# Optimization experiments

Hardware: AMD Instinct MI355X
Metric: run time of the kernel (lower is better)

## Reference

```python
import jax, jax.numpy as jnp
import numpy as np

L, H, D, DH, F = 2, 12, 768, 64, 3072
B, T = 2, 2048
LN_EPS = 1e-5


def setup_inputs() -> dict:
    key = jax.random.key(0)
    ks = jax.random.split(key, 16)
    s = 0.02
    inp = {
        "x": jax.random.normal(ks[0], (B, T, D), dtype=jnp.float32),
        "attn_mask": jnp.ones((1, T, T), dtype=jnp.int32),
        # per-layer, per-head QKV projections
        "Wq": jax.random.normal(ks[1], (L, H, D, DH), jnp.float32) * s,
        "bq": jnp.zeros((L, H, DH), jnp.float32),
        "Wk": jax.random.normal(ks[2], (L, H, D, DH), jnp.float32) * s,
        "bk": jnp.zeros((L, H, DH), jnp.float32),
        "Wv": jax.random.normal(ks[3], (L, H, D, DH), jnp.float32) * s,
        "bv": jnp.zeros((L, H, DH), jnp.float32),
        # output projection over concatenated heads
        "Wo": jax.random.normal(ks[4], (L, H * DH, D), jnp.float32) * s,
        "bo": jnp.zeros((L, D), jnp.float32),
        # FFN: LayerNorm -> Linear -> GELU -> Linear
        "ln_g": jnp.ones((L, D), jnp.float32),
        "ln_b": jnp.zeros((L, D), jnp.float32),
        "W1": jax.random.normal(ks[5], (L, D, F), jnp.float32) * s,
        "b1": jnp.zeros((L, F), jnp.float32),
        "W2": jax.random.normal(ks[6], (L, F, D), jnp.float32) * s,
        "b2": jnp.zeros((L, D), jnp.float32),
    }
    return inp


def _layer(x, mask, Wq, bq, Wk, bk, Wv, bv, Wo, bo, ln_g, ln_b, W1, b1, W2, b2):
    # batched multi-head attention (equivalent to per-head loop in source)
    q = jnp.einsum("btd,hde->bhte", x, Wq) + bq[None, :, None, :]
    k = jnp.einsum("btd,hde->bhte", x, Wk) + bk[None, :, None, :]
    v = jnp.einsum("btd,hde->bhte", x, Wv) + bv[None, :, None, :]
    scores = jnp.einsum("bhte,bhse->bhts", q, k) / np.sqrt(DH).astype(np.float32)
    scores = jnp.where(mask[:, None, :, :] == 0, -jnp.inf, scores)
    alpha = jax.nn.softmax(scores, axis=-1)
    attn = jnp.einsum("bhts,bhse->bhte", alpha, v)  # [B,H,T,DH]
    concat = attn.transpose(0, 2, 1, 3).reshape(x.shape[0], x.shape[1], H * DH)
    x = concat @ Wo + bo + x  # attention residual
    # FFN with pre-LayerNorm inside the block, residual around it
    mu = jnp.mean(x, axis=-1, keepdims=True)
    var = jnp.mean(jnp.square(x - mu), axis=-1, keepdims=True)
    h = (x - mu) * jax.lax.rsqrt(var + LN_EPS) * ln_g + ln_b
    h = jax.nn.gelu(h @ W1 + b1, approximate=False) @ W2 + b2
    return h + x


def reference(x, attn_mask, Wq, bq, Wk, bk, Wv, bv, Wo, bo, ln_g, ln_b, W1, b1, W2, b2):
    for l in range(L):
        x = _layer(x, attn_mask,
                   Wq[l], bq[l], Wk[l], bk[l], Wv[l], bv[l],
                   Wo[l], bo[l], ln_g[l], ln_b[l],
                   W1[l], b1[l], W2[l], b2[l])
    return x
```

## Files before the change

### kernel.cpp

```cpp
#include <hip/hip_runtime.h>
#include <math.h>

#define CL 2
#define CH 12
#define CD 768
#define CDH 64
#define CF 3072
#define CB 2
#define CT 2048
#define CBTCD ((size_t)CB * CT * CD)

typedef __bf16 bf16x8 __attribute__((ext_vector_type(8)));
typedef float f32x4 __attribute__((ext_vector_type(4)));
typedef short s16x4 __attribute__((ext_vector_type(4)));
typedef ushort u16x4 __attribute__((ext_vector_type(4)));

#define QSCALE 0.18033688011112042f

__device__ __forceinline__ ushort f2bf(float f) {
  return __builtin_bit_cast(ushort, (__bf16)f);
}

__device__ __forceinline__ float fexp2(float x) {
  float r;
  asm volatile("v_exp_f32 %0, %1" : "=v"(r) : "v"(x));
  return r;
}

__device__ __forceinline__ float wred_sum(float v) {
#pragma unroll
  for (int o = 32; o > 0; o >>= 1) v += __shfl_xor(v, o);
  return v;
}

__device__ __forceinline__ void gload16(const ushort* g, ushort* l) {
  __builtin_amdgcn_global_load_lds(
      (const __attribute__((address_space(1))) unsigned int*)g,
      (__attribute__((address_space(3))) unsigned int*)l, 16, 0, 0);
}

enum { EPI_BF16 = 1, EPI_BIAS_BF16 = 2, EPI_BIAS_GELU_BF16 = 3, EPI_BIAS_RES_F32 = 4, EPI_BIAS_RES_F32_BF16 = 5, EPI_PART_F32 = 6 };

template <int EPI>
__global__ __launch_bounds__(256) void gemm_k(
    const ushort* __restrict__ A, int lda,
    const ushort* __restrict__ B, int ldb,
    void* __restrict__ Cv, int ldc,
    int K,
    const float* __restrict__ bias,
    const float* __restrict__ res,
    ushort* __restrict__ C2) {
  __shared__ ushort As[2][128 * 32];
  __shared__ ushort Bs[2][128 * 32];
  const int tid = threadIdx.x;
  const int lane = tid & 63;
  const int wave = tid >> 6;
  const int wm = (wave >> 1) * 64;
  const int wn = (wave & 1) * 64;

  const int gx = gridDim.x;
  const int nwg = gx * gridDim.y;
  int wgid = blockIdx.y * gx + blockIdx.x;
  const int cpx = nwg >> 3;
  wgid = (wgid & 7) * cpx + (wgid >> 3);
  const int m0 = (wgid / gx) * 128;
  const int n0 = (wgid % gx) * 128;

  const int lr = lane & 15;
  const int lg = lane >> 4;
  f32x4 acc[4][4] = {};

  const int kz = blockIdx.z * K;
  const ushort* pa = A + (size_t)(m0 + (tid >> 2)) * lda + (tid & 3) * 8 + kz;
  const ushort* pb = B + (size_t)(n0 + (tid >> 2)) * ldb + (tid & 3) * 8 + kz;

  auto stage = [&](int buf, int k0) {
#pragma unroll
    for (int p = 0; p < 2; ++p) {
      gload16(pa + (size_t)p * 64 * lda + k0, &As[buf][wave * 512 + p * 2048]);
      gload16(pb + (size_t)p * 64 * ldb + k0, &Bs[buf][wave * 512 + p * 2048]);
    }
  };

  const int nt = K >> 5;
  stage(0, 0);
  for (int kt = 0; kt < nt; ++kt) {
    const int cur = kt & 1;
    if (kt + 1 < nt) {
      stage(cur ^ 1, (kt + 1) << 5);
      asm volatile("s_waitcnt vmcnt(4)" ::: "memory");
    } else {
      asm volatile("s_waitcnt vmcnt(0)" ::: "memory");
    }
    __builtin_amdgcn_s_barrier();
    __builtin_amdgcn_sched_barrier(0);

    bf16x8 af[4], bfr[4];
#pragma unroll
    for (int f = 0; f < 4; ++f) af[f] = *(const bf16x8*)(&As[cur][(wm + f * 16 + lr) * 32 + lg * 8]);
#pragma unroll
    for (int f = 0; f < 4; ++f) bfr[f] = *(const bf16x8*)(&Bs[cur][(wn + f * 16 + lr) * 32 + lg * 8]);
#pragma unroll
    for (int i = 0; i < 4; ++i)
#pragma unroll
      for (int j = 0; j < 4; ++j)
        acc[i][j] = __builtin_amdgcn_mfma_f32_16x16x32_bf16(af[i], bfr[j], acc[i][j], 0, 0, 0);

    __builtin_amdgcn_sched_barrier(0);
    __builtin_amdgcn_s_barrier();
  }

  const int cr0 = lg * 4;
#pragma unroll
  for (int i = 0; i < 4; ++i) {
#pragma unroll
    for (int j = 0; j < 4; ++j) {
      int col = n0 + wn + j * 16 + lr;
#pragma unroll
      for (int r = 0; r < 4; ++r) {
        int row = m0 + wm + i * 16 + cr0 + r;
        float val = acc[i][j][r];
        size_t offc = (size_t)row * ldc + col;
        if constexpr (EPI == EPI_BF16) {
          ((ushort*)Cv)[offc] = f2bf(val);
        } else if constexpr (EPI == EPI_BIAS_BF16) {
          ((ushort*)Cv)[offc] = f2bf(val + bias[col]);
        } else if constexpr (EPI == EPI_BIAS_GELU_BF16) {
          float x = val + bias[col];
          float gel = 0.5f * x * (1.0f + erff(x * 0.70710678118654752f));
          ((ushort*)Cv)[offc] = f2bf(gel);
        } else if constexpr (EPI == EPI_BIAS_RES_F32) {
          ((float*)Cv)[offc] = val + bias[col] + res[offc];
        } else if constexpr (EPI == EPI_PART_F32) {
          ((float*)Cv)[blockIdx.z * CBTCD + offc] = val;
        } else {
          float o = val + bias[col] + res[offc];
          ((float*)Cv)[offc] = o;
          C2[offc] = f2bf(o);
        }
      }
    }
  }
}

template <bool DUAL>
__global__ __launch_bounds__(256) void reduce2_k(const float* __restrict__ part,
                                                 const float* __restrict__ bias,
                                                 const float* __restrict__ res,
                                                 float* __restrict__ outf,
                                                 ushort* __restrict__ outb) {
  int i = blockIdx.x * 256 + threadIdx.x;
  float4 p0 = ((const float4*)part)[i];
  float4 p1 = ((const float4*)(part + CBTCD))[i];
  float4 rr = ((const float4*)res)[i];
  int col = (i * 4) % CD;
  float4 bb = *(const float4*)(bias + col);
  float4 o;
  o.x = p0.x + p1.x + rr.x + bb.x;
  o.y = p0.y + p1.y + rr.y + bb.y;
  o.z = p0.z + p1.z + rr.z + bb.z;
  o.w = p0.w + p1.w + rr.w + bb.w;
  ((float4*)outf)[i] = o;
  if constexpr (DUAL) {
    ushort4 u;
    u.x = f2bf(o.x); u.y = f2bf(o.y); u.z = f2bf(o.z); u.w = f2bf(o.w);
    ((ushort4*)outb)[i] = u;
  }
}

__global__ __launch_bounds__(256) void flash_k(const ushort* __restrict__ qkv,
                                               const ushort* __restrict__ vt,
                                               const unsigned* __restrict__ mbits,
                                               ushort* __restrict__ out) {
  const int q0 = blockIdx.x * 64;
  const int bh = blockIdx.y;
  const int b = bh / CH, h = bh % CH;
  const int tid = threadIdx.x;
  const int lane = tid & 63;
  const int wave = tid >> 6;
  const int lr = lane & 15;
  const int lg = lane >> 4;

  __shared__ ushort Ks[64][72];
  __shared__ ushort Vt[64][72];

  const int qg = q0 + wave * 16 + lr;
  const ushort* qrow = qkv + ((size_t)(b * CT) + qg) * 2304 + h * CDH;
  bf16x8 aq0 = *(const bf16x8*)(qrow + lg * 8);
  bf16x8 aq1 = *(const bf16x8*)(qrow + 32 + lg * 8);

  f32x4 acc[4] = {};
  float m_run = -1e30f, l_run = 0.f;

  const ushort* kbase = qkv + (size_t)(b * CT) * 2304 + CD + h * CDH;
  const ushort* vbase = vt + (size_t)bh * 64 * CT;

  for (int kv0 = 0; kv0 < CT; kv0 += 64) {
    __syncthreads();
#pragma unroll
    for (int p = 0; p < 2; ++p) {
      int i = p * 2048 + tid * 8;
      int r = i >> 6, c = i & 63;
      *(bf16x8*)(&Ks[r][c]) = *(const bf16x8*)(kbase + (size_t)(kv0 + r) * 2304 + c);
      *(bf16x8*)(&Vt[r][c]) = *(const bf16x8*)(vbase + (size_t)r * CT + kv0 + c);
    }
    __syncthreads();

    f32x4 st[4];
    __builtin_amdgcn_s_setprio(1);
#pragma unroll
    for (int j = 0; j < 4; ++j) {
      bf16x8 kf0 = *(const bf16x8*)(&Ks[j * 16 + lr][lg * 8]);
      bf16x8 kf1 = *(const bf16x8*)(&Ks[j * 16 + lr][32 + lg * 8]);
      f32x4 t = {};
      t = __builtin_amdgcn_mfma_f32_16x16x32_bf16(kf0, aq0, t, 0, 0, 0);
      t = __builtin_amdgcn_mfma_f32_16x16x32_bf16(kf1, aq1, t, 0, 0, 0);
      st[j] = t;
    }
    __builtin_amdgcn_s_setprio(0);

    unsigned w0 = mbits[(size_t)qg * 64 + (kv0 >> 5)];
    unsigned w1 = mbits[(size_t)qg * 64 + (kv0 >> 5) + 1];
    float tmax = -INFINITY;
    if ((w0 & w1) == 0xFFFFFFFFu) {
#pragma unroll
      for (int j = 0; j < 4; ++j)
#pragma unroll
        for (int r = 0; r < 4; ++r) tmax = fmaxf(tmax, st[j][r]);
    } else {
#pragma unroll
      for (int j = 0; j < 4; ++j) {
        unsigned w = (j < 2) ? w0 : w1;
#pragma unroll
        for (int r = 0; r < 4; ++r) {
          int bit = (j * 16 + lg * 4 + r) & 31;
          if (((w >> bit) & 1u) == 0u) st[j][r] = -INFINITY;
          tmax = fmaxf(tmax, st[j][r]);
        }
      }
    }
    tmax = fmaxf(tmax, __shfl_xor(tmax, 16));
    tmax = fmaxf(tmax, __shfl_xor(tmax, 32));

    if (__any(tmax - m_run > 8.0f)) {
      float mnew = fmaxf(m_run, tmax);
      float sc = fexp2(m_run - mnew);
      m_run = mnew;
      l_run *= sc;
#pragma unroll
      for (int jj = 0; jj < 4; ++jj) {
        acc[jj][0] *= sc; acc[jj][1] *= sc; acc[jj][2] *= sc; acc[jj][3] *= sc;
      }
    }

    float tsum = 0.f;
    s16x4 pf[4];
#pragma unroll
    for (int j = 0; j < 4; ++j) {
      s16x4 pv;
#pragma unroll
      for (int r = 0; r < 4; ++r) {
        float p = fexp2(st[j][r] - m_run);
        tsum += p;
        pv[r] = (short)f2bf(p);
      }
      pf[j] = pv;
    }
    tsum += __shfl_xor(tsum, 16);
    tsum += __shfl_xor(tsum, 32);
    l_run += tsum;

    __builtin_amdgcn_s_setprio(1);
#pragma unroll
    for (int jj = 0; jj < 4; ++jj) {
#pragma unroll
      for (int j = 0; j < 4; ++j) {
        s16x4 vf = *(const s16x4*)(&Vt[jj * 16 + lr][j * 16 + lg * 4]);
        acc[jj] = __builtin_amdgcn_mfma_f32_16x16x16bf16_1k(vf, pf[j], acc[jj], 0, 0, 0);
      }
    }
    __builtin_amdgcn_s_setprio(0);
  }

  float inv = 1.0f / l_run;
  const int orow = b * CT + qg;
#pragma unroll
  for (int jj = 0; jj < 4; ++jj) {
    u16x4 o;
#pragma unroll
    for (int r = 0; r < 4; ++r) o[r] = f2bf(acc[jj][r] * inv);
    *(u16x4*)(out + (size_t)orow * CD + h * CDH + jj * 16 + lg * 4) = o;
  }
}

__global__ __launch_bounds__(256) void vtrans_k(const ushort* __restrict__ qkv,
                                                ushort* __restrict__ vt) {
  const int t0 = blockIdx.x * 64;
  const int bh = blockIdx.y;
  const int b = bh / CH, h = bh % CH;
  const int tid = threadIdx.x;
  __shared__ ushort tile[64][72];
#pragma unroll
  for (int p = 0; p < 2; ++p) {
    int i = p * 2048 + tid * 8;
    int tr = i >> 6, c = i & 63;
    *(bf16x8*)(&tile[tr][c]) =
        *(const bf16x8*)(qkv + (size_t)(b * CT + t0 + tr) * 2304 + 2 * CD + h * CDH + c);
  }
  __syncthreads();
#pragma unroll
  for (int p = 0; p < 2; ++p) {
    int i = p * 2048 + tid * 8;
    int er = i >> 6, tc = i & 63;
    ushort tmp[8];
#pragma unroll
    for (int j = 0; j < 8; ++j) tmp[j] = tile[tc + j][er];
    *(bf16x8*)(vt + (size_t)bh * 64 * CT + (size_t)er * CT + t0 + tc) = *(bf16x8*)tmp;
  }
}

__global__ void maskbits_k(const int* __restrict__ mask, unsigned* __restrict__ mbits) {
  int idx = blockIdx.x * 256 + threadIdx.x;
  if (idx >= CT * 64) return;
  const int* mp = mask + (size_t)(idx >> 6) * CT + (idx & 63) * 32;
  unsigned bits = 0;
#pragma unroll
  for (int j = 0; j < 32; ++j) bits |= (mp[j] != 0 ? 1u : 0u) << j;
  mbits[idx] = bits;
}

__global__ __launch_bounds__(256) void ln_k(const float* __restrict__ X,
                                            ushort* __restrict__ H,
                                            const float* __restrict__ g,
                                            const float* __restrict__ b) {
  const int t = blockIdx.x;
  const int tid = threadIdx.x;
  const float* row = X + (size_t)t * CD;
  float x0 = row[tid], x1 = row[tid + 256], x2 = row[tid + 512];
  float s = wred_sum(x0 + x1 + x2);
  __shared__ float sh[4], sh2[4];
  if ((tid & 63) == 0) sh[tid >> 6] = s;
  __syncthreads();
  float mu = (sh[0] + sh[1] + sh[2] + sh[3]) * (1.0f / 768.0f);
  float d0 = x0 - mu, d1 = x1 - mu, d2 = x2 - mu;
  float vs = wred_sum(d0 * d0 + d1 * d1 + d2 * d2);
  if ((tid & 63) == 0) sh2[tid >> 6] = vs;
  __syncthreads();
  float var = (sh2[0] + sh2[1] + sh2[2] + sh2[3]) * (1.0f / 768.0f);
  float r = 1.0f / sqrtf(var + 1e-5f);
  H[(size_t)t * CD + tid] = f2bf(d0 * r * g[tid] + b[tid]);
  H[(size_t)t * CD + tid + 256] = f2bf(d1 * r * g[tid + 256] + b[tid + 256]);
  H[(size_t)t * CD + tid + 512] = f2bf(d2 * r * g[tid + 512] + b[tid + 512]);
}

__global__ void f32_to_bf16_k(const float* __restrict__ in, ushort* __restrict__ out, int n4) {
  int i = blockIdx.x * 256 + threadIdx.x;
  if (i >= n4) return;
  float4 f = *(const float4*)(in + (size_t)i * 4);
  ushort4 u;
  u.x = f2bf(f.x); u.y = f2bf(f.y); u.z = f2bf(f.z); u.w = f2bf(f.w);
  *(ushort4*)(out + (size_t)i * 4) = u;
}

__global__ __launch_bounds__(256) void tcvt_k(const float* __restrict__ src, size_t sbs,
                                              ushort* __restrict__ dst, size_t dbs,
                                              int R, int C, float scale) {
  __shared__ float t[32][33];
  const float* s = src + blockIdx.z * sbs;
  ushort* d = dst + blockIdx.z * dbs;
  const int tx = threadIdx.x & 31;
  const int ty4 = (threadIdx.x >> 5) * 4;
  const int r0 = blockIdx.y * 32, c0 = blockIdx.x * 32;
#pragma unroll
  for (int i = 0; i < 4; ++i) t[ty4 + i][tx] = s[(size_t)(r0 + ty4 + i) * C + c0 + tx];
  __syncthreads();
#pragma unroll
  for (int i = 0; i < 4; ++i)
    d[(size_t)(c0 + ty4 + i) * R + r0 + tx] = f2bf(t[tx][ty4 + i] * scale);
}

__global__ void repack_bqkv_k(const float* __restrict__ bq, const float* __restrict__ bk,
                              const float* __restrict__ bv, float* __restrict__ dst) {
  int idx = blockIdx.x * 256 + threadIdx.x;
  if (idx >= CL * 2304) return;
  int l = idx / 2304;
  int c = idx % 2304;
  int sec = c / CD;
  int within = c % CD;
  int h = within / CDH;
  int e = within % CDH;
  const float* B = (sec == 0) ? bq : ((sec == 1) ? bk : bv);
  float v = B[((size_t)l * CH + h) * CDH + e];
  if (sec == 0) v *= QSCALE;
  dst[idx] = v;
}

extern "C" void kernel_launch(void* const* d_in, const int* in_sizes, int n_in,
                              void* d_out, int out_size, void* d_ws, size_t ws_size,
                              hipStream_t stream) {
  (void)in_sizes; (void)n_in; (void)out_size; (void)ws_size;
  const float* X = (const float*)d_in[0];
  const int* MSK = (const int*)d_in[1];
  const float* Wq = (const float*)d_in[2];
  const float* bq = (const float*)d_in[3];
  const float* Wk = (const float*)d_in[4];
  const float* bk = (const float*)d_in[5];
  const float* Wv = (const float*)d_in[6];
  const float* bv = (const float*)d_in[7];
  const float* Wo = (const float*)d_in[8];
  const float* bo = (const float*)d_in[9];
  const float* lng = (const float*)d_in[10];
  const float* lnb = (const float*)d_in[11];
  const float* W1 = (const float*)d_in[12];
  const float* b1 = (const float*)d_in[13];
  const float* W2 = (const float*)d_in[14];
  const float* b2 = (const float*)d_in[15];

  char* base = (char*)d_ws;
  size_t off = 0;
  auto alloc = [&](size_t bytes) {
    char* p = base + off;
    off = (off + bytes + 255) & ~(size_t)255;
    return p;
  };
  ushort* wqkv_t = (ushort*)alloc((size_t)CL * 2304 * CD * 2);
  ushort* wo_t = (ushort*)alloc((size_t)CL * CD * CD * 2);
  ushort* w1_t = (ushort*)alloc((size_t)CL * CF * CD * 2);
  ushort* w2_t = (ushort*)alloc((size_t)CL * CD * CF * 2);
  float* bqkv = (float*)alloc((size_t)CL * 2304 * 4);
  ushort* xb = (ushort*)alloc((size_t)CB * CT * CD * 2);
  ushort* qkv = (ushort*)alloc((size_t)CB * CT * 2304 * 2);
  ushort* vt = (ushort*)alloc((size_t)CB * CH * CDH * CT * 2);
  unsigned* mbits = (unsigned*)alloc((size_t)CT * 64 * 4);
  ushort* attno = (ushort*)alloc((size_t)CB * CT * CD * 2);
  float* xattn = (float*)alloc((size_t)CB * CT * CD * 4);
  float* xf = (float*)alloc((size_t)CB * CT * CD * 4);
  ushort* hln = (ushort*)alloc((size_t)CB * CT * CD * 2);
  ushort* gbuf = (ushort*)alloc((size_t)CB * CT * CF * 2);
  float* part = (float*)qkv;

  const int BT_ = CB * CT;

  for (int l = 0; l < CL; ++l) {
    tcvt_k<<<dim3(CDH / 32, CD / 32, CH), 256, 0, stream>>>(
        Wq + (size_t)l * CH * CD * CDH, (size_t)CD * CDH,
        wqkv_t + (size_t)l * 2304 * CD + 0 * CD * CD, (size_t)CDH * CD,
        CD, CDH, QSCALE);
    tcvt_k<<<dim3(CDH / 32, CD / 32, CH), 256, 0, stream>>>(
        Wk + (size_t)l * CH * CD * CDH, (size_t)CD * CDH,
        wqkv_t + (size_t)l * 2304 * CD + 1 * CD * CD, (size_t)CDH * CD,
        CD, CDH, 1.0f);
    tcvt_k<<<dim3(CDH / 32, CD / 32, CH), 256, 0, stream>>>(
        Wv + (size_t)l * CH * CD * CDH, (size_t)CD * CDH,
        wqkv_t + (size_t)l * 2304 * CD + 2 * CD * CD, (size_t)CDH * CD,
        CD, CDH, 1.0f);
  }
  tcvt_k<<<dim3(CD / 32, CD / 32, CL), 256, 0, stream>>>(
      Wo, (size_t)CD * CD, wo_t, (size_t)CD * CD, CD, CD, 1.0f);
  tcvt_k<<<dim3(CF / 32, CD / 32, CL), 256, 0, stream>>>(
      W1, (size_t)CD * CF, w1_t, (size_t)CF * CD, CD, CF, 1.0f);
  tcvt_k<<<dim3(CD / 32, CF / 32, CL), 256, 0, stream>>>(
      W2, (size_t)CF * CD, w2_t, (size_t)CD * CF, CF, CD, 1.0f);
  {
    int n = CL * 2304;
    repack_bqkv_k<<<(n + 255) / 256, 256, 0, stream>>>(bq, bk, bv, bqkv);
  }
  maskbits_k<<<(CT * 64 + 255) / 256, 256, 0, stream>>>(MSK, mbits);

  {
    int n4 = BT_ * CD / 4;
    f32_to_bf16_k<<<(n4 + 255) / 256, 256, 0, stream>>>(X, xb, n4);
  }

  for (int l = 0; l < CL; ++l) {
    const float* xcur = (l == 0) ? X : xf;
    gemm_k<EPI_BIAS_BF16><<<dim3(2304 / 128, BT_ / 128), 256, 0, stream>>>(
        xb, CD, wqkv_t + (size_t)l * 2304 * CD, CD, qkv, 2304, CD,
        bqkv + (size_t)l * 2304, nullptr, nullptr);
    vtrans_k<<<dim3(CT / 64, CB * CH), 256, 0, stream>>>(qkv, vt);
    flash_k<<<dim3(CT / 64, CB * CH), 256, 0, stream>>>(qkv, vt, mbits, attno);
    gemm_k<EPI_BIAS_RES_F32><<<dim3(CD / 128, BT_ / 128), 256, 0, stream>>>(
        attno, CD, wo_t + (size_t)l * CD * CD, CD, xattn, CD, CD,
        bo + (size_t)l * CD, xcur, nullptr);
    ln_k<<<BT_, 256, 0, stream>>>(xattn, hln, lng + (size_t)l * CD, lnb + (size_t)l * CD);
    gemm_k<EPI_BIAS_GELU_BF16><<<dim3(CF / 128, BT_ / 128), 256, 0, stream>>>(
        hln, CD, w1_t + (size_t)l * CF * CD, CD, gbuf, CF, CD,
        b1 + (size_t)l * CF, nullptr, nullptr);
    gemm_k<EPI_PART_F32><<<dim3(CD / 128, BT_ / 128, 2), 256, 0, stream>>>(
        gbuf, CF, w2_t + (size_t)l * CD * CF, CF, part, CD, CF / 2,
        nullptr, nullptr, nullptr);
    const int nred = BT_ * CD / 4 / 256;
    if (l == CL - 1) {
      reduce2_k<false><<<nred, 256, 0, stream>>>(part, b2 + (size_t)l * CD, xattn,
                                                 (float*)d_out, nullptr);
    } else {
      reduce2_k<true><<<nred, 256, 0, stream>>>(part, b2 + (size_t)l * CD, xattn,
                                                xf, xb);
    }
  }
}
```

Measured before the change: 440.3 us.

## Prefetch next K/V tile into registers while computing current attention tile

The flash-attention loop now loads the next 64-row K and V tiles from global memory into registers before computing on the current shared-memory tile, giving a register double-buffer that hides global load latency behind the MFMA work. It also defers the cross-lane reduction of the softmax row sum until after the loop, dropping two shuffles per tile. The cost is higher register pressure from the extra prefetch registers. Correctness of the deferred sum relies on every rescale being applied uniformly across lanes, and it is.

```diff
diff --git a/kernel.cpp b/kernel.cpp
--- a/kernel.cpp
+++ b/kernel.cpp
@@ -195,18 +195,23 @@
   const ushort* kbase = qkv + (size_t)(b * CT) * 2304 + CD + h * CDH;
   const ushort* vbase = vt + (size_t)bh * 64 * CT;
 
-  for (int kv0 = 0; kv0 < CT; kv0 += 64) {
-    __syncthreads();
-#pragma unroll
-    for (int p = 0; p < 2; ++p) {
-      int i = p * 2048 + tid * 8;
-      int r = i >> 6, c = i & 63;
-      *(bf16x8*)(&Ks[r][c]) = *(const bf16x8*)(kbase + (size_t)(kv0 + r) * 2304 + c);
-      *(bf16x8*)(&Vt[r][c]) = *(const bf16x8*)(vbase + (size_t)r * CT + kv0 + c);
-    }
-    __syncthreads();
-
-    f32x4 st[4];
+  const int r0 = tid >> 3, r1 = 32 + (tid >> 3), cc = (tid & 7) * 8;
+
+  auto ld = [&](int kv0, bf16x8& k0, bf16x8& k1, bf16x8& v0, bf16x8& v1) {
+    k0 = *(const bf16x8*)(kbase + (size_t)(kv0 + r0) * 2304 + cc);
+    k1 = *(const bf16x8*)(kbase + (size_t)(kv0 + r1) * 2304 + cc);
+    v0 = *(const bf16x8*)(vbase + (size_t)r0 * CT + kv0 + cc);
+    v1 = *(const bf16x8*)(vbase + (size_t)r1 * CT + kv0 + cc);
+  };
+  auto st = [&](bf16x8 k0, bf16x8 k1, bf16x8 v0, bf16x8 v1) {
+    *(bf16x8*)(&Ks[r0][cc]) = k0;
+    *(bf16x8*)(&Ks[r1][cc]) = k1;
+    *(bf16x8*)(&Vt[r0][cc]) = v0;
+    *(bf16x8*)(&Vt[r1][cc]) = v1;
+  };
+
+  auto compute = [&](int kv0) {
+    f32x4 stt[4];
     __builtin_amdgcn_s_setprio(1);
 #pragma unroll
     for (int j = 0; j < 4; ++j) {
@@ -215,7 +220,7 @@
       f32x4 t = {};
       t = __builtin_amdgcn_mfma_f32_16x16x32_bf16(kf0, aq0, t, 0, 0, 0);
       t = __builtin_amdgcn_mfma_f32_16x16x32_bf16(kf1, aq1, t, 0, 0, 0);
-      st[j] = t;
+      stt[j] = t;
     }
     __builtin_amdgcn_s_setprio(0);
 
@@ -226,7 +231,7 @@
 #pragma unroll
       for (int j = 0; j < 4; ++j)
 #pragma unroll
-        for (int r = 0; r < 4; ++r) tmax = fmaxf(tmax, st[j][r]);
+        for (int r = 0; r < 4; ++r) tmax = fmaxf(tmax, stt[j][r]);
     } else {
 #pragma unroll
       for (int j = 0; j < 4; ++j) {
@@ -234,8 +239,8 @@
 #pragma unroll
         for (int r = 0; r < 4; ++r) {
           int bit = (j * 16 + lg * 4 + r) & 31;
-          if (((w >> bit) & 1u) == 0u) st[j][r] = -INFINITY;
-          tmax = fmaxf(tmax, st[j][r]);
+          if (((w >> bit) & 1u) == 0u) stt[j][r] = -INFINITY;
+          tmax = fmaxf(tmax, stt[j][r]);
         }
       }
     }
@@ -253,22 +258,18 @@
       }
     }
 
-    float tsum = 0.f;
     s16x4 pf[4];
 #pragma unroll
     for (int j = 0; j < 4; ++j) {
       s16x4 pv;
 #pragma unroll
       for (int r = 0; r < 4; ++r) {
-        float p = fexp2(st[j][r] - m_run);
-        tsum += p;
+        float p = fexp2(stt[j][r] - m_run);
+        l_run += p;
         pv[r] = (short)f2bf(p);
       }
       pf[j] = pv;
     }
-    tsum += __shfl_xor(tsum, 16);
-    tsum += __shfl_xor(tsum, 32);
-    l_run += tsum;
 
     __builtin_amdgcn_s_setprio(1);
 #pragma unroll
@@ -280,7 +281,25 @@
       }
     }
     __builtin_amdgcn_s_setprio(0);
-  }
+  };
+
+  bf16x8 ka0, ka1, va0, va1, kb0, kb1, vb0, vb1;
+  ld(0, ka0, ka1, va0, va1);
+  for (int kv0 = 0; kv0 < CT; kv0 += 128) {
+    __syncthreads();
+    st(ka0, ka1, va0, va1);
+    __syncthreads();
+    ld(kv0 + 64, kb0, kb1, vb0, vb1);
+    compute(kv0);
+    __syncthreads();
+    st(kb0, kb1, vb0, vb1);
+    __syncthreads();
+    if (kv0 + 128 < CT) ld(kv0 + 128, ka0, ka1, va0, va1);
+    compute(kv0 + 64);
+  }
+
+  l_run += __shfl_xor(l_run, 16);
+  l_run += __shfl_xor(l_run, 32);
 
   float inv = 1.0f / l_run;
   const int orow = b * CT + qg;
```

Measured after the change: 438.5 us. Within noise of the previous version (-0.4%).
